# Kernel tuning notes

Measured on AMD Instinct MI355X. Metric: run time of the kernel, lower is better.

Reference implementation:

```python
import jax, jax.numpy as jnp
import numpy as np

ALIGN_CORNERS = True
APPLY_SMOOTHSTEP = True

SIZES = [(32, 32, 32), (64, 64, 64), (128, 128, 128), (256, 256, 256)]
FEAT_DIMS = [4, 4, 4, 4]
N_POINTS = 1048576  # 2**20 sample points (e.g. 8192 rays x 128 samples)


def setup_inputs() -> dict:
    key = jax.random.key(0)
    ks = jax.random.split(key, 1 + len(SIZES))
    # grid_sample-style coords in [-1, 1], layout [1, 1, 1, N, 3] (x, y, z)
    grid = jax.random.uniform(ks[0], (1, 1, 1, N_POINTS, 3), dtype=jnp.float32) * 2.0 - 1.0
    inp = {"grid": grid}
    for i, (size, c) in enumerate(zip(SIZES, FEAT_DIMS)):
        # original init: (rand(1,C,1,1,1)*2-1).repeat over spatial; use randn volumes for a
        # non-degenerate baseline (same shapes/math path)
        inp[f"vol{i}"] = jax.random.normal(ks[1 + i], (1, c, *size), dtype=jnp.float32)
    return inp


def _smooth_sample(vol, grid_pts):
    """Trilinear sample with border padding, align_corners=True, smoothstep weights.

    vol: [C, D, H, W]; grid_pts: [P, 3] with (x, y, z) in [-1, 1].
    Returns [C, P].
    """
    C, D, H, W = vol.shape
    # unnormalize (align_corners=True): [-1,1] -> [0, dim-1]; border padding via clip
    x = jnp.clip((grid_pts[:, 0] + 1.0) * 0.5 * (W - 1), 0.0, W - 1)
    y = jnp.clip((grid_pts[:, 1] + 1.0) * 0.5 * (H - 1), 0.0, H - 1)
    z = jnp.clip((grid_pts[:, 2] + 1.0) * 0.5 * (D - 1), 0.0, D - 1)

    x0 = jnp.floor(x); y0 = jnp.floor(y); z0 = jnp.floor(z)
    tx = x - x0; ty = y - y0; tz = z - z0
    if APPLY_SMOOTHSTEP:
        tx = tx * tx * (3.0 - 2.0 * tx)
        ty = ty * ty * (3.0 - 2.0 * ty)
        tz = tz * tz * (3.0 - 2.0 * tz)

    x0i = x0.astype(jnp.int32); x1i = jnp.minimum(x0i + 1, W - 1)
    y0i = y0.astype(jnp.int32); y1i = jnp.minimum(y0i + 1, H - 1)
    z0i = z0.astype(jnp.int32); z1i = jnp.minimum(z0i + 1, D - 1)

    # 8 corner gathers -> [C, P]
    c000 = vol[:, z0i, y0i, x0i]; c001 = vol[:, z0i, y0i, x1i]
    c010 = vol[:, z0i, y1i, x0i]; c011 = vol[:, z0i, y1i, x1i]
    c100 = vol[:, z1i, y0i, x0i]; c101 = vol[:, z1i, y0i, x1i]
    c110 = vol[:, z1i, y1i, x0i]; c111 = vol[:, z1i, y1i, x1i]

    c00 = c000 + (c001 - c000) * tx
    c01 = c010 + (c011 - c010) * tx
    c10 = c100 + (c101 - c100) * tx
    c11 = c110 + (c111 - c110) * tx
    c0 = c00 + (c01 - c00) * ty
    c1 = c10 + (c11 - c10) * ty
    return c0 + (c1 - c0) * tz


def reference(grid, vol0, vol1, vol2, vol3):
    # grid: [1, 1, 1, N, 3] -> [N, 3]
    pts = grid.reshape(-1, 3)
    n = pts.shape[0]
    out = []
    for vol in (vol0, vol1, vol2, vol3):
        feat = _smooth_sample(vol[0], pts)            # [C, N]
        out.append(feat.reshape(1, -1, 1, 1, n))      # grid_sample output layout
    return jnp.concatenate(out, axis=1)               # [1, sum(C), 1, 1, N]
```

## Files before the change

kernel.cpp:

```cpp
#include <hip/hip_runtime.h>

#define NPTS 1048576
#define NB 32
#define NBINS (NB * NB * NB)

typedef float v4f __attribute__((ext_vector_type(4)));

__device__ __forceinline__ void nt_store4(const float4& f, float4* p) {
    __builtin_nontemporal_store(*(const v4f*)&f, (v4f*)p);
}


__device__ __forceinline__ float4 lerp4(const float4 a, const float4 b, const float t) {
    return make_float4(a.x + (b.x - a.x) * t,
                       a.y + (b.y - a.y) * t,
                       a.z + (b.z - a.z) * t,
                       a.w + (b.w - a.w) * t);
}

struct CoordW { float tx, ty, tz; int b00, b01, b10, b11, x0, x1; };

template<int D>
__device__ __forceinline__ CoordW mkcoord(float gx, float gy, float gz) {
    CoordW c;
    float x = fminf(fmaxf((gx + 1.0f) * (0.5f * (float)(D - 1)), 0.0f), (float)(D - 1));
    float y = fminf(fmaxf((gy + 1.0f) * (0.5f * (float)(D - 1)), 0.0f), (float)(D - 1));
    float z = fminf(fmaxf((gz + 1.0f) * (0.5f * (float)(D - 1)), 0.0f), (float)(D - 1));
    float xf = floorf(x), yf = floorf(y), zf = floorf(z);
    float tx = x - xf, ty = y - yf, tz = z - zf;
    c.tx = tx * tx * (3.0f - 2.0f * tx);
    c.ty = ty * ty * (3.0f - 2.0f * ty);
    c.tz = tz * tz * (3.0f - 2.0f * tz);
    int x0 = (int)xf, y0 = (int)yf, z0 = (int)zf;
    int y1 = min(y0 + 1, D - 1), z1 = min(z0 + 1, D - 1);
    c.x0 = x0;
    c.x1 = min(x0 + 1, D - 1);
    c.b00 = (z0 * D + y0) * D;
    c.b01 = (z0 * D + y1) * D;
    c.b10 = (z1 * D + y0) * D;
    c.b11 = (z1 * D + y1) * D;
    return c;
}

__device__ __forceinline__ float4 reduce8(const float4* q, const CoordW& c) {
    float4 c00 = lerp4(q[0], q[1], c.tx);
    float4 c01 = lerp4(q[2], q[3], c.tx);
    float4 c10 = lerp4(q[4], q[5], c.tx);
    float4 c11 = lerp4(q[6], q[7], c.tx);
    float4 c0 = lerp4(c00, c01, c.ty);
    float4 c1 = lerp4(c10, c11, c.ty);
    return lerp4(c0, c1, c.tz);
}


#define DHW0 (32 * 32 * 32)
#define DHW1 (64 * 64 * 64)
#define DHW2 (128 * 128 * 128)

__global__ __launch_bounds__(256) void xpose_all_kernel(
    const float* __restrict__ v0, const float* __restrict__ v1, const float* __restrict__ v2,
    float4* __restrict__ w0, float4* __restrict__ w1, float4* __restrict__ w2)
{
    constexpr int B2 = DHW2 / 256, B1 = DHW1 / 256;
    int b = blockIdx.x;
    int t = threadIdx.x;
    if (b < B2) {
        int v = b * 256 + t;
        w2[v] = make_float4(v2[v], v2[v + DHW2], v2[v + 2 * DHW2], v2[v + 3 * DHW2]);
    } else if (b < B2 + B1) {
        int v = (b - B2) * 256 + t;
        w1[v] = make_float4(v1[v], v1[v + DHW1], v1[v + 2 * DHW1], v1[v + 3 * DHW1]);
    } else {
        int v = (b - B2 - B1) * 256 + t;
        w0[v] = make_float4(v0[v], v0[v + DHW0], v0[v + 2 * DHW0], v0[v + 3 * DHW0]);
    }
}


__device__ __forceinline__ int bin_of(float gx, float gy, float gz) {
    float ux = fminf(fmaxf((gx + 1.0f) * 0.5f, 0.0f), 1.0f);
    float uy = fminf(fmaxf((gy + 1.0f) * 0.5f, 0.0f), 1.0f);
    float uz = fminf(fmaxf((gz + 1.0f) * 0.5f, 0.0f), 1.0f);
    int bx = min((int)(ux * (float)NB), NB - 1);
    int by = min((int)(uy * (float)NB), NB - 1);
    int bz = min((int)(uz * (float)NB), NB - 1);
    return (bz * NB + by) * NB + bx;
}

__global__ __launch_bounds__(256) void bin_hist_kernel(const float* __restrict__ grid,
                                                       unsigned* __restrict__ hist) {
    int p = blockIdx.x * blockDim.x + threadIdx.x;
    float gx = grid[3 * p + 0];
    float gy = grid[3 * p + 1];
    float gz = grid[3 * p + 2];
    atomicAdd(&hist[bin_of(gx, gy, gz)], 1u);
}

__global__ __launch_bounds__(1024) void scan_kernel(const unsigned* __restrict__ hist,
                                                    unsigned* __restrict__ offsets) {
    __shared__ unsigned partial[1024];
    const int t = threadIdx.x;
    const int base = t * 32;
    unsigned sum = 0;
#pragma unroll
    for (int i = 0; i < 32; ++i) sum += hist[base + i];
    partial[t] = sum;
    __syncthreads();
    for (int off = 1; off < 1024; off <<= 1) {
        unsigned v = (t >= off) ? partial[t - off] : 0u;
        __syncthreads();
        partial[t] += v;
        __syncthreads();
    }
    unsigned run = partial[t] - sum;
#pragma unroll
    for (int i = 0; i < 32; ++i) {
        offsets[base + i] = run;
        run += hist[base + i];
    }
}

__global__ __launch_bounds__(256) void scatter_kernel(const float* __restrict__ grid,
                                                      unsigned* __restrict__ offsets,
                                                      float4* __restrict__ sorted,
                                                      int* __restrict__ inv) {
    int p = blockIdx.x * blockDim.x + threadIdx.x;
    float gx = grid[3 * p + 0];
    float gy = grid[3 * p + 1];
    float gz = grid[3 * p + 2];
    int b = bin_of(gx, gy, gz);
    unsigned pos = atomicAdd(&offsets[b], 1u);
    sorted[pos] = make_float4(gx, gy, gz, __int_as_float(p));
    inv[p] = (int)pos;
}


__global__ __launch_bounds__(256, 4) void gather_sorted_kernel(
    const float4* __restrict__ sorted,
    const float4* __restrict__ w0, const float4* __restrict__ w1,
    const float4* __restrict__ w2, const float* __restrict__ v3,
    float4* __restrict__ wsout)
{
    int bid = blockIdx.x;
    int sb = (bid & 7) * (int)(gridDim.x >> 3) + (bid >> 3);
    int s = sb * 256 + (int)threadIdx.x;
    float4 gp = sorted[s];
    float gx = gp.x, gy = gp.y, gz = gp.z;

    CoordW c0 = mkcoord<32>(gx, gy, gz);
    CoordW c1 = mkcoord<64>(gx, gy, gz);
    CoordW c2 = mkcoord<128>(gx, gy, gz);
    CoordW c3 = mkcoord<256>(gx, gy, gz);

    float4 qa[8], qb[8], qc[8];
    qa[0] = w0[c0.b00 + c0.x0]; qa[1] = w0[c0.b00 + c0.x1];
    qa[2] = w0[c0.b01 + c0.x0]; qa[3] = w0[c0.b01 + c0.x1];
    qa[4] = w0[c0.b10 + c0.x0]; qa[5] = w0[c0.b10 + c0.x1];
    qa[6] = w0[c0.b11 + c0.x0]; qa[7] = w0[c0.b11 + c0.x1];

    qb[0] = w1[c1.b00 + c1.x0]; qb[1] = w1[c1.b00 + c1.x1];
    qb[2] = w1[c1.b01 + c1.x0]; qb[3] = w1[c1.b01 + c1.x1];
    qb[4] = w1[c1.b10 + c1.x0]; qb[5] = w1[c1.b10 + c1.x1];
    qb[6] = w1[c1.b11 + c1.x0]; qb[7] = w1[c1.b11 + c1.x1];

    qc[0] = w2[c2.b00 + c2.x0]; qc[1] = w2[c2.b00 + c2.x1];
    qc[2] = w2[c2.b01 + c2.x0]; qc[3] = w2[c2.b01 + c2.x1];
    qc[4] = w2[c2.b10 + c2.x0]; qc[5] = w2[c2.b10 + c2.x1];
    qc[6] = w2[c2.b11 + c2.x0]; qc[7] = w2[c2.b11 + c2.x1];

    const int xm = min(c3.x0, 254);
    const bool edge = (c3.x0 == 255);
    float2 qd[16];
#pragma unroll
    for (int ch = 0; ch < 4; ++ch) {
        const float* __restrict__ vc = v3 + (size_t)ch * (256 * 256 * 256);
        qd[ch * 4 + 0] = *(const float2*)(vc + c3.b00 + xm);
        qd[ch * 4 + 1] = *(const float2*)(vc + c3.b01 + xm);
        qd[ch * 4 + 2] = *(const float2*)(vc + c3.b10 + xm);
        qd[ch * 4 + 3] = *(const float2*)(vc + c3.b11 + xm);
    }

    float4 f0 = reduce8(qa, c0);
    float4 f1 = reduce8(qb, c1);
    float4 f2 = reduce8(qc, c2);

    float r3[4];
#pragma unroll
    for (int ch = 0; ch < 4; ++ch) {
        float v00a = edge ? qd[ch * 4 + 0].y : qd[ch * 4 + 0].x, v00b = qd[ch * 4 + 0].y;
        float v01a = edge ? qd[ch * 4 + 1].y : qd[ch * 4 + 1].x, v01b = qd[ch * 4 + 1].y;
        float v10a = edge ? qd[ch * 4 + 2].y : qd[ch * 4 + 2].x, v10b = qd[ch * 4 + 2].y;
        float v11a = edge ? qd[ch * 4 + 3].y : qd[ch * 4 + 3].x, v11b = qd[ch * 4 + 3].y;
        float c00 = v00a + (v00b - v00a) * c3.tx;
        float c01 = v01a + (v01b - v01a) * c3.tx;
        float c10 = v10a + (v10b - v10a) * c3.tx;
        float c11 = v11a + (v11b - v11a) * c3.tx;
        float e0 = c00 + (c01 - c00) * c3.ty;
        float e1 = c10 + (c11 - c10) * c3.ty;
        r3[ch] = e0 + (e1 - e0) * c3.tz;
    }
    float4 f3 = make_float4(r3[0], r3[1], r3[2], r3[3]);

    float4* w = wsout + (size_t)s * 4;
    nt_store4(f0, w + 0);
    nt_store4(f1, w + 1);
    nt_store4(f2, w + 2);
    nt_store4(f3, w + 3);
}


__device__ __forceinline__ void permute_one(const float4* __restrict__ wsout,
                                            const int* __restrict__ inv,
                                            float* __restrict__ out, int p) {
    int s = inv[p];
    const float4* w = wsout + (size_t)s * 4;
    float4 f0 = w[0], f1 = w[1], f2 = w[2], f3 = w[3];
    __builtin_nontemporal_store(f0.x, &out[ 0 * NPTS + p]);
    __builtin_nontemporal_store(f0.y, &out[ 1 * NPTS + p]);
    __builtin_nontemporal_store(f0.z, &out[ 2 * NPTS + p]);
    __builtin_nontemporal_store(f0.w, &out[ 3 * NPTS + p]);
    __builtin_nontemporal_store(f1.x, &out[ 4 * NPTS + p]);
    __builtin_nontemporal_store(f1.y, &out[ 5 * NPTS + p]);
    __builtin_nontemporal_store(f1.z, &out[ 6 * NPTS + p]);
    __builtin_nontemporal_store(f1.w, &out[ 7 * NPTS + p]);
    __builtin_nontemporal_store(f2.x, &out[ 8 * NPTS + p]);
    __builtin_nontemporal_store(f2.y, &out[ 9 * NPTS + p]);
    __builtin_nontemporal_store(f2.z, &out[10 * NPTS + p]);
    __builtin_nontemporal_store(f2.w, &out[11 * NPTS + p]);
    __builtin_nontemporal_store(f3.x, &out[12 * NPTS + p]);
    __builtin_nontemporal_store(f3.y, &out[13 * NPTS + p]);
    __builtin_nontemporal_store(f3.z, &out[14 * NPTS + p]);
    __builtin_nontemporal_store(f3.w, &out[15 * NPTS + p]);
}

__global__ __launch_bounds__(256) void permute_kernel(const float4* __restrict__ wsout,
                                                      const int* __restrict__ inv,
                                                      float* __restrict__ out) {
    int p = blockIdx.x * blockDim.x + threadIdx.x;
    permute_one(wsout, inv, out, p);
    permute_one(wsout, inv, out, p + NPTS / 2);
}


template<int D>
__device__ __forceinline__ float4 sample_inter(const float4* __restrict__ v,
                                               float gx, float gy, float gz) {
    CoordW c = mkcoord<D>(gx, gy, gz);
    float4 q[8];
    q[0] = v[c.b00 + c.x0]; q[1] = v[c.b00 + c.x1];
    q[2] = v[c.b01 + c.x0]; q[3] = v[c.b01 + c.x1];
    q[4] = v[c.b10 + c.x0]; q[5] = v[c.b10 + c.x1];
    q[6] = v[c.b11 + c.x0]; q[7] = v[c.b11 + c.x1];
    return reduce8(q, c);
}

template<int D>
__device__ __forceinline__ float4 sample_direct(const float* __restrict__ v,
                                                float gx, float gy, float gz) {
    CoordW c = mkcoord<D>(gx, gy, gz);
    float r[4];
#pragma unroll
    for (int ch = 0; ch < 4; ++ch) {
        const float* __restrict__ vc = v + (size_t)ch * (D * D * D);
        float c000 = vc[c.b00 + c.x0], c001 = vc[c.b00 + c.x1];
        float c010 = vc[c.b01 + c.x0], c011 = vc[c.b01 + c.x1];
        float c100 = vc[c.b10 + c.x0], c101 = vc[c.b10 + c.x1];
        float c110 = vc[c.b11 + c.x0], c111 = vc[c.b11 + c.x1];
        float c00 = c000 + (c001 - c000) * c.tx;
        float c01 = c010 + (c011 - c010) * c.tx;
        float c10 = c100 + (c101 - c100) * c.tx;
        float c11 = c110 + (c111 - c110) * c.tx;
        float e0 = c00 + (c01 - c00) * c.ty;
        float e1 = c10 + (c11 - c10) * c.ty;
        r[ch] = e0 + (e1 - e0) * c.tz;
    }
    return make_float4(r[0], r[1], r[2], r[3]);
}

__global__ __launch_bounds__(256) void mg_direct_kernel(
    const float* __restrict__ grid,
    const float* __restrict__ v0, const float* __restrict__ v1,
    const float* __restrict__ v2, const float* __restrict__ v3,
    float* __restrict__ out)
{
    int p = blockIdx.x * blockDim.x + threadIdx.x;
    float gx = grid[3 * p + 0];
    float gy = grid[3 * p + 1];
    float gz = grid[3 * p + 2];
    float4 f0 = sample_direct<32>(v0, gx, gy, gz);
    float4 f1 = sample_direct<64>(v1, gx, gy, gz);
    float4 f2 = sample_direct<128>(v2, gx, gy, gz);
    float4 f3 = sample_direct<256>(v3, gx, gy, gz);
    out[ 0 * NPTS + p] = f0.x; out[ 1 * NPTS + p] = f0.y;
    out[ 2 * NPTS + p] = f0.z; out[ 3 * NPTS + p] = f0.w;
    out[ 4 * NPTS + p] = f1.x; out[ 5 * NPTS + p] = f1.y;
    out[ 6 * NPTS + p] = f1.z; out[ 7 * NPTS + p] = f1.w;
    out[ 8 * NPTS + p] = f2.x; out[ 9 * NPTS + p] = f2.y;
    out[10 * NPTS + p] = f2.z; out[11 * NPTS + p] = f2.w;
    out[12 * NPTS + p] = f3.x; out[13 * NPTS + p] = f3.y;
    out[14 * NPTS + p] = f3.z; out[15 * NPTS + p] = f3.w;
}

__global__ __launch_bounds__(256) void mg_inter_kernel(
    const float* __restrict__ grid,
    const float4* __restrict__ w0, const float4* __restrict__ w1,
    const float4* __restrict__ w2, const float* __restrict__ v3,
    float* __restrict__ out)
{
    int p = blockIdx.x * blockDim.x + threadIdx.x;
    float gx = grid[3 * p + 0];
    float gy = grid[3 * p + 1];
    float gz = grid[3 * p + 2];
    float4 f0 = sample_inter<32>(w0, gx, gy, gz);
    float4 f1 = sample_inter<64>(w1, gx, gy, gz);
    float4 f2 = sample_inter<128>(w2, gx, gy, gz);
    float4 f3 = sample_direct<256>(v3, gx, gy, gz);
    out[ 0 * NPTS + p] = f0.x; out[ 1 * NPTS + p] = f0.y;
    out[ 2 * NPTS + p] = f0.z; out[ 3 * NPTS + p] = f0.w;
    out[ 4 * NPTS + p] = f1.x; out[ 5 * NPTS + p] = f1.y;
    out[ 6 * NPTS + p] = f1.z; out[ 7 * NPTS + p] = f1.w;
    out[ 8 * NPTS + p] = f2.x; out[ 9 * NPTS + p] = f2.y;
    out[10 * NPTS + p] = f2.z; out[11 * NPTS + p] = f2.w;
    out[12 * NPTS + p] = f3.x; out[13 * NPTS + p] = f3.y;
    out[14 * NPTS + p] = f3.z; out[15 * NPTS + p] = f3.w;
}


extern "C" void kernel_launch(void* const* d_in, const int* in_sizes, int n_in,
                              void* d_out, int out_size, void* d_ws, size_t ws_size,
                              hipStream_t stream) {
    const float* grid = (const float*)d_in[0];
    const float* v0   = (const float*)d_in[1];
    const float* v1   = (const float*)d_in[2];
    const float* v2   = (const float*)d_in[3];
    const float* v3   = (const float*)d_in[4];
    float* out = (float*)d_out;

    constexpr size_t OFF_WSOUT  = 0;
    constexpr size_t OFF_SORTED = OFF_WSOUT  + (size_t)NPTS * 64;
    constexpr size_t OFF_W2     = OFF_SORTED + (size_t)NPTS * 16;
    constexpr size_t OFF_W1     = OFF_W2     + (size_t)DHW2 * 16;
    constexpr size_t OFF_W0     = OFF_W1     + (size_t)DHW1 * 16;
    constexpr size_t OFF_INV    = OFF_W0     + (size_t)DHW0 * 16;
    constexpr size_t OFF_HIST   = OFF_INV    + (size_t)NPTS * 4;
    constexpr size_t OFF_OFFS   = OFF_HIST   + (size_t)NBINS * 4;
    constexpr size_t WS_FULL    = OFF_OFFS   + (size_t)NBINS * 4;
    constexpr size_t WS_INTER   = (size_t)(DHW0 + DHW1 + DHW2) * 16;

    const int threads = 256;
    const int pt_blocks = NPTS / threads;
    char* ws = (char*)d_ws;

    if (ws_size >= WS_FULL) {
        float4*   wsout  = (float4*)(ws + OFF_WSOUT);
        float4*   sorted = (float4*)(ws + OFF_SORTED);
        float4*   w2     = (float4*)(ws + OFF_W2);
        float4*   w1     = (float4*)(ws + OFF_W1);
        float4*   w0     = (float4*)(ws + OFF_W0);
        int*      inv    = (int*)   (ws + OFF_INV);
        unsigned* hist   = (unsigned*)(ws + OFF_HIST);
        unsigned* offs   = (unsigned*)(ws + OFF_OFFS);

        (void)hipMemsetAsync(hist, 0, (size_t)NBINS * 4, stream);
        xpose_all_kernel<<<(DHW0 + DHW1 + DHW2) / threads, threads, 0, stream>>>(
            v0, v1, v2, w0, w1, w2);
        bin_hist_kernel<<<pt_blocks, threads, 0, stream>>>(grid, hist);
        scan_kernel<<<1, 1024, 0, stream>>>(hist, offs);
        scatter_kernel<<<pt_blocks, threads, 0, stream>>>(grid, offs, sorted, inv);
        gather_sorted_kernel<<<pt_blocks, threads, 0, stream>>>(sorted, w0, w1, w2, v3, wsout);
        permute_kernel<<<pt_blocks / 2, threads, 0, stream>>>(wsout, inv, out);
    } else if (ws_size >= WS_INTER) {
        float4* w0 = (float4*)d_ws;
        float4* w1 = w0 + DHW0;
        float4* w2 = w1 + DHW1;
        xpose_all_kernel<<<(DHW0 + DHW1 + DHW2) / threads, threads, 0, stream>>>(
            v0, v1, v2, w0, w1, w2);
        mg_inter_kernel<<<pt_blocks, threads, 0, stream>>>(grid, w0, w1, w2, v3, out);
    } else {
        mg_direct_kernel<<<pt_blocks, threads, 0, stream>>>(grid, v0, v1, v2, v3, out);
    }
}
```

Baseline: 662.8 us.

## Fuse transpose with histogram, scatter results by original index, drop inverse map

Merges the volume transpose and bin-histogram kernels into one launch. The gather kernel now writes each point's results at its original index, taken from the packed sorted record, so the inverse-index array and its indirect read in the final permute go away. The final pass becomes a straight coalesced read and transpose. The gather kernel also gets a scheduling barrier after its loads and its occupancy hint drops from 4 to 3; the workspace writes become scattered rather than sequential.

```diff
diff --git a/kernel.cpp b/kernel.cpp
--- a/kernel.cpp
+++ b/kernel.cpp
@@ -4,9 +4,14 @@
 #define NB 32
 #define NBINS (NB * NB * NB)
 
+#define DHW0 (32 * 32 * 32)
+#define DHW1 (64 * 64 * 64)
+#define DHW2 (128 * 128 * 128)
+#define DHW3 (256 * 256 * 256)
+
 typedef float v4f __attribute__((ext_vector_type(4)));
 
-__device__ __forceinline__ void nt_store4(const float4& f, float4* p) {
+__device__ __forceinline__ void nt_store4(const float4 f, float4* p) {
     __builtin_nontemporal_store(*(const v4f*)&f, (v4f*)p);
 }
 
@@ -52,16 +57,43 @@
     return lerp4(c0, c1, c.tz);
 }
 
-
-#define DHW0 (32 * 32 * 32)
-#define DHW1 (64 * 64 * 64)
-#define DHW2 (128 * 128 * 128)
-
-__global__ __launch_bounds__(256) void xpose_all_kernel(
+__device__ __forceinline__ float4 reduce_v3(const float2* qd, const CoordW& c, bool edge) {
+    float r[4];
+#pragma unroll
+    for (int ch = 0; ch < 4; ++ch) {
+        float v00a = edge ? qd[ch * 4 + 0].y : qd[ch * 4 + 0].x, v00b = qd[ch * 4 + 0].y;
+        float v01a = edge ? qd[ch * 4 + 1].y : qd[ch * 4 + 1].x, v01b = qd[ch * 4 + 1].y;
+        float v10a = edge ? qd[ch * 4 + 2].y : qd[ch * 4 + 2].x, v10b = qd[ch * 4 + 2].y;
+        float v11a = edge ? qd[ch * 4 + 3].y : qd[ch * 4 + 3].x, v11b = qd[ch * 4 + 3].y;
+        float c00 = v00a + (v00b - v00a) * c.tx;
+        float c01 = v01a + (v01b - v01a) * c.tx;
+        float c10 = v10a + (v10b - v10a) * c.tx;
+        float c11 = v11a + (v11b - v11a) * c.tx;
+        float e0 = c00 + (c01 - c00) * c.ty;
+        float e1 = c10 + (c11 - c10) * c.ty;
+        r[ch] = e0 + (e1 - e0) * c.tz;
+    }
+    return make_float4(r[0], r[1], r[2], r[3]);
+}
+
+
+__device__ __forceinline__ int bin_of(float gx, float gy, float gz) {
+    float ux = fminf(fmaxf((gx + 1.0f) * 0.5f, 0.0f), 1.0f);
+    float uy = fminf(fmaxf((gy + 1.0f) * 0.5f, 0.0f), 1.0f);
+    float uz = fminf(fmaxf((gz + 1.0f) * 0.5f, 0.0f), 1.0f);
+    int bx = min((int)(ux * (float)NB), NB - 1);
+    int by = min((int)(uy * (float)NB), NB - 1);
+    int bz = min((int)(uz * (float)NB), NB - 1);
+    return (bz * NB + by) * NB + bx;
+}
+
+
+__global__ __launch_bounds__(256) void xpose_hist_kernel(
     const float* __restrict__ v0, const float* __restrict__ v1, const float* __restrict__ v2,
-    float4* __restrict__ w0, float4* __restrict__ w1, float4* __restrict__ w2)
+    float4* __restrict__ w0, float4* __restrict__ w1, float4* __restrict__ w2,
+    const float* __restrict__ grid, unsigned* __restrict__ hist)
 {
-    constexpr int B2 = DHW2 / 256, B1 = DHW1 / 256;
+    constexpr int B2 = DHW2 / 256, B1 = DHW1 / 256, B0 = DHW0 / 256;
     int b = blockIdx.x;
     int t = threadIdx.x;
     if (b < B2) {
@@ -70,30 +102,16 @@
     } else if (b < B2 + B1) {
         int v = (b - B2) * 256 + t;
         w1[v] = make_float4(v1[v], v1[v + DHW1], v1[v + 2 * DHW1], v1[v + 3 * DHW1]);
-    } else {
+    } else if (b < B2 + B1 + B0) {
         int v = (b - B2 - B1) * 256 + t;
         w0[v] = make_float4(v0[v], v0[v + DHW0], v0[v + 2 * DHW0], v0[v + 3 * DHW0]);
-    }
-}
-
-
-__device__ __forceinline__ int bin_of(float gx, float gy, float gz) {
-    float ux = fminf(fmaxf((gx + 1.0f) * 0.5f, 0.0f), 1.0f);
-    float uy = fminf(fmaxf((gy + 1.0f) * 0.5f, 0.0f), 1.0f);
-    float uz = fminf(fmaxf((gz + 1.0f) * 0.5f, 0.0f), 1.0f);
-    int bx = min((int)(ux * (float)NB), NB - 1);
-    int by = min((int)(uy * (float)NB), NB - 1);
-    int bz = min((int)(uz * (float)NB), NB - 1);
-    return (bz * NB + by) * NB + bx;
-}
-
-__global__ __launch_bounds__(256) void bin_hist_kernel(const float* __restrict__ grid,
-                                                       unsigned* __restrict__ hist) {
-    int p = blockIdx.x * blockDim.x + threadIdx.x;
-    float gx = grid[3 * p + 0];
-    float gy = grid[3 * p + 1];
-    float gz = grid[3 * p + 2];
-    atomicAdd(&hist[bin_of(gx, gy, gz)], 1u);
+    } else {
+        int p = (b - B2 - B1 - B0) * 256 + t;
+        float gx = grid[3 * p + 0];
+        float gy = grid[3 * p + 1];
+        float gz = grid[3 * p + 2];
+        atomicAdd(&hist[bin_of(gx, gy, gz)], 1u);
+    }
 }
 
 __global__ __launch_bounds__(1024) void scan_kernel(const unsigned* __restrict__ hist,
@@ -122,8 +140,7 @@
 
 __global__ __launch_bounds__(256) void scatter_kernel(const float* __restrict__ grid,
                                                       unsigned* __restrict__ offsets,
-                                                      float4* __restrict__ sorted,
-                                                      int* __restrict__ inv) {
+                                                      float4* __restrict__ sorted) {
     int p = blockIdx.x * blockDim.x + threadIdx.x;
     float gx = grid[3 * p + 0];
     float gy = grid[3 * p + 1];
@@ -131,11 +148,10 @@
     int b = bin_of(gx, gy, gz);
     unsigned pos = atomicAdd(&offsets[b], 1u);
     sorted[pos] = make_float4(gx, gy, gz, __int_as_float(p));
-    inv[p] = (int)pos;
-}
-
-
-__global__ __launch_bounds__(256, 4) void gather_sorted_kernel(
+}
+
+
+__global__ __launch_bounds__(256, 3) void gather_sorted_kernel(
     const float4* __restrict__ sorted,
     const float4* __restrict__ w0, const float4* __restrict__ w1,
     const float4* __restrict__ w2, const float* __restrict__ v3,
@@ -146,13 +162,18 @@
     int s = sb * 256 + (int)threadIdx.x;
     float4 gp = sorted[s];
     float gx = gp.x, gy = gp.y, gz = gp.z;
+    int origP = __float_as_int(gp.w);
 
     CoordW c0 = mkcoord<32>(gx, gy, gz);
     CoordW c1 = mkcoord<64>(gx, gy, gz);
     CoordW c2 = mkcoord<128>(gx, gy, gz);
     CoordW c3 = mkcoord<256>(gx, gy, gz);
+    const int  xm = min(c3.x0, 254);
+    const bool edge = (c3.x0 == 255);
 
     float4 qa[8], qb[8], qc[8];
+    float2 qd[16];
+
     qa[0] = w0[c0.b00 + c0.x0]; qa[1] = w0[c0.b00 + c0.x1];
     qa[2] = w0[c0.b01 + c0.x0]; qa[3] = w0[c0.b01 + c0.x1];
     qa[4] = w0[c0.b10 + c0.x0]; qa[5] = w0[c0.b10 + c0.x1];
@@ -168,40 +189,23 @@
     qc[4] = w2[c2.b10 + c2.x0]; qc[5] = w2[c2.b10 + c2.x1];
     qc[6] = w2[c2.b11 + c2.x0]; qc[7] = w2[c2.b11 + c2.x1];
 
-    const int xm = min(c3.x0, 254);
-    const bool edge = (c3.x0 == 255);
-    float2 qd[16];
 #pragma unroll
     for (int ch = 0; ch < 4; ++ch) {
-        const float* __restrict__ vc = v3 + (size_t)ch * (256 * 256 * 256);
+        const float* __restrict__ vc = v3 + (size_t)ch * DHW3;
         qd[ch * 4 + 0] = *(const float2*)(vc + c3.b00 + xm);
         qd[ch * 4 + 1] = *(const float2*)(vc + c3.b01 + xm);
         qd[ch * 4 + 2] = *(const float2*)(vc + c3.b10 + xm);
         qd[ch * 4 + 3] = *(const float2*)(vc + c3.b11 + xm);
     }
 
+    __builtin_amdgcn_sched_barrier(0);
+
     float4 f0 = reduce8(qa, c0);
     float4 f1 = reduce8(qb, c1);
     float4 f2 = reduce8(qc, c2);
-
-    float r3[4];
-#pragma unroll
-    for (int ch = 0; ch < 4; ++ch) {
-        float v00a = edge ? qd[ch * 4 + 0].y : qd[ch * 4 + 0].x, v00b = qd[ch * 4 + 0].y;
-        float v01a = edge ? qd[ch * 4 + 1].y : qd[ch * 4 + 1].x, v01b = qd[ch * 4 + 1].y;
-        float v10a = edge ? qd[ch * 4 + 2].y : qd[ch * 4 + 2].x, v10b = qd[ch * 4 + 2].y;
-        float v11a = edge ? qd[ch * 4 + 3].y : qd[ch * 4 + 3].x, v11b = qd[ch * 4 + 3].y;
-        float c00 = v00a + (v00b - v00a) * c3.tx;
-        float c01 = v01a + (v01b - v01a) * c3.tx;
-        float c10 = v10a + (v10b - v10a) * c3.tx;
-        float c11 = v11a + (v11b - v11a) * c3.tx;
-        float e0 = c00 + (c01 - c00) * c3.ty;
-        float e1 = c10 + (c11 - c10) * c3.ty;
-        r3[ch] = e0 + (e1 - e0) * c3.tz;
-    }
-    float4 f3 = make_float4(r3[0], r3[1], r3[2], r3[3]);
-
-    float4* w = wsout + (size_t)s * 4;
+    float4 f3 = reduce_v3(qd, c3, edge);
+
+    float4* w = wsout + (size_t)origP * 4;
     nt_store4(f0, w + 0);
     nt_store4(f1, w + 1);
     nt_store4(f2, w + 2);
@@ -209,11 +213,10 @@
 }
 
 
-__device__ __forceinline__ void permute_one(const float4* __restrict__ wsout,
-                                            const int* __restrict__ inv,
-                                            float* __restrict__ out, int p) {
-    int s = inv[p];
-    const float4* w = wsout + (size_t)s * 4;
+__global__ __launch_bounds__(256) void unpermute_kernel(const float4* __restrict__ wsout,
+                                                        float* __restrict__ out) {
+    int p = blockIdx.x * blockDim.x + threadIdx.x;
+    const float4* w = wsout + (size_t)p * 4;
     float4 f0 = w[0], f1 = w[1], f2 = w[2], f3 = w[3];
     __builtin_nontemporal_store(f0.x, &out[ 0 * NPTS + p]);
     __builtin_nontemporal_store(f0.y, &out[ 1 * NPTS + p]);
@@ -233,14 +236,6 @@
     __builtin_nontemporal_store(f3.w, &out[15 * NPTS + p]);
 }
 
-__global__ __launch_bounds__(256) void permute_kernel(const float4* __restrict__ wsout,
-                                                      const int* __restrict__ inv,
-                                                      float* __restrict__ out) {
-    int p = blockIdx.x * blockDim.x + threadIdx.x;
-    permute_one(wsout, inv, out, p);
-    permute_one(wsout, inv, out, p + NPTS / 2);
-}
-
 
 template<int D>
 __device__ __forceinline__ float4 sample_inter(const float4* __restrict__ v,
@@ -275,6 +270,19 @@
         r[ch] = e0 + (e1 - e0) * c.tz;
     }
     return make_float4(r[0], r[1], r[2], r[3]);
+}
+
+__device__ __forceinline__ void store16(const float4 f0, const float4 f1,
+                                        const float4 f2, const float4 f3,
+                                        float* __restrict__ out, int p) {
+    out[ 0 * NPTS + p] = f0.x; out[ 1 * NPTS + p] = f0.y;
+    out[ 2 * NPTS + p] = f0.z; out[ 3 * NPTS + p] = f0.w;
+    out[ 4 * NPTS + p] = f1.x; out[ 5 * NPTS + p] = f1.y;
+    out[ 6 * NPTS + p] = f1.z; out[ 7 * NPTS + p] = f1.w;
+    out[ 8 * NPTS + p] = f2.x; out[ 9 * NPTS + p] = f2.y;
+    out[10 * NPTS + p] = f2.z; out[11 * NPTS + p] = f2.w;
+    out[12 * NPTS + p] = f3.x; out[13 * NPTS + p] = f3.y;
+    out[14 * NPTS + p] = f3.z; out[15 * NPTS + p] = f3.w;
 }
 
 __global__ __launch_bounds__(256) void mg_direct_kernel(
@@ -291,14 +299,7 @@
     float4 f1 = sample_direct<64>(v1, gx, gy, gz);
     float4 f2 = sample_direct<128>(v2, gx, gy, gz);
     float4 f3 = sample_direct<256>(v3, gx, gy, gz);
-    out[ 0 * NPTS + p] = f0.x; out[ 1 * NPTS + p] = f0.y;
-    out[ 2 * NPTS + p] = f0.z; out[ 3 * NPTS + p] = f0.w;
-    out[ 4 * NPTS + p] = f1.x; out[ 5 * NPTS + p] = f1.y;
-    out[ 6 * NPTS + p] = f1.z; out[ 7 * NPTS + p] = f1.w;
-    out[ 8 * NPTS + p] = f2.x; out[ 9 * NPTS + p] = f2.y;
-    out[10 * NPTS + p] = f2.z; out[11 * NPTS + p] = f2.w;
-    out[12 * NPTS + p] = f3.x; out[13 * NPTS + p] = f3.y;
-    out[14 * NPTS + p] = f3.z; out[15 * NPTS + p] = f3.w;
+    store16(f0, f1, f2, f3, out, p);
 }
 
 __global__ __launch_bounds__(256) void mg_inter_kernel(
@@ -315,14 +316,7 @@
     float4 f1 = sample_inter<64>(w1, gx, gy, gz);
     float4 f2 = sample_inter<128>(w2, gx, gy, gz);
     float4 f3 = sample_direct<256>(v3, gx, gy, gz);
-    out[ 0 * NPTS + p] = f0.x; out[ 1 * NPTS + p] = f0.y;
-    out[ 2 * NPTS + p] = f0.z; out[ 3 * NPTS + p] = f0.w;
-    out[ 4 * NPTS + p] = f1.x; out[ 5 * NPTS + p] = f1.y;
-    out[ 6 * NPTS + p] = f1.z; out[ 7 * NPTS + p] = f1.w;
-    out[ 8 * NPTS + p] = f2.x; out[ 9 * NPTS + p] = f2.y;
-    out[10 * NPTS + p] = f2.z; out[11 * NPTS + p] = f2.w;
-    out[12 * NPTS + p] = f3.x; out[13 * NPTS + p] = f3.y;
-    out[14 * NPTS + p] = f3.z; out[15 * NPTS + p] = f3.w;
+    store16(f0, f1, f2, f3, out, p);
 }
 
 
@@ -341,8 +335,7 @@
     constexpr size_t OFF_W2     = OFF_SORTED + (size_t)NPTS * 16;
     constexpr size_t OFF_W1     = OFF_W2     + (size_t)DHW2 * 16;
     constexpr size_t OFF_W0     = OFF_W1     + (size_t)DHW1 * 16;
-    constexpr size_t OFF_INV    = OFF_W0     + (size_t)DHW0 * 16;
-    constexpr size_t OFF_HIST   = OFF_INV    + (size_t)NPTS * 4;
+    constexpr size_t OFF_HIST   = OFF_W0     + (size_t)DHW0 * 16;
     constexpr size_t OFF_OFFS   = OFF_HIST   + (size_t)NBINS * 4;
     constexpr size_t WS_FULL    = OFF_OFFS   + (size_t)NBINS * 4;
     constexpr size_t WS_INTER   = (size_t)(DHW0 + DHW1 + DHW2) * 16;
@@ -357,24 +350,24 @@
         float4*   w2     = (float4*)(ws + OFF_W2);
         float4*   w1     = (float4*)(ws + OFF_W1);
         float4*   w0     = (float4*)(ws + OFF_W0);
-        int*      inv    = (int*)   (ws + OFF_INV);
         unsigned* hist   = (unsigned*)(ws + OFF_HIST);
         unsigned* offs   = (unsigned*)(ws + OFF_OFFS);
 
         (void)hipMemsetAsync(hist, 0, (size_t)NBINS * 4, stream);
-        xpose_all_kernel<<<(DHW0 + DHW1 + DHW2) / threads, threads, 0, stream>>>(
-            v0, v1, v2, w0, w1, w2);
-        bin_hist_kernel<<<pt_blocks, threads, 0, stream>>>(grid, hist);
+        const int xh_blocks = (DHW0 + DHW1 + DHW2) / threads + pt_blocks;
+        xpose_hist_kernel<<<xh_blocks, threads, 0, stream>>>(
+            v0, v1, v2, w0, w1, w2, grid, hist);
         scan_kernel<<<1, 1024, 0, stream>>>(hist, offs);
-        scatter_kernel<<<pt_blocks, threads, 0, stream>>>(grid, offs, sorted, inv);
-        gather_sorted_kernel<<<pt_blocks, threads, 0, stream>>>(sorted, w0, w1, w2, v3, wsout);
-        permute_kernel<<<pt_blocks / 2, threads, 0, stream>>>(wsout, inv, out);
+        scatter_kernel<<<pt_blocks, threads, 0, stream>>>(grid, offs, sorted);
+        gather_sorted_kernel<<<pt_blocks, threads, 0, stream>>>(
+            sorted, w0, w1, w2, v3, wsout);
+        unpermute_kernel<<<pt_blocks, threads, 0, stream>>>(wsout, out);
     } else if (ws_size >= WS_INTER) {
         float4* w0 = (float4*)d_ws;
         float4* w1 = w0 + DHW0;
         float4* w2 = w1 + DHW1;
-        xpose_all_kernel<<<(DHW0 + DHW1 + DHW2) / threads, threads, 0, stream>>>(
-            v0, v1, v2, w0, w1, w2);
+        xpose_hist_kernel<<<(DHW0 + DHW1 + DHW2) / threads, threads, 0, stream>>>(
+            v0, v1, v2, w0, w1, w2, grid, (unsigned*)nullptr);
         mg_inter_kernel<<<pt_blocks, threads, 0, stream>>>(grid, w0, w1, w2, v3, out);
     } else {
         mg_direct_kernel<<<pt_blocks, threads, 0, stream>>>(grid, v0, v1, v2, v3, out);
```

Measured after the change: 743.5 us. 12.2% more time.
